# Optimization experiments

Measured on AMD Instinct MI355X. Metric: run time of the kernel, lower is better.

## Reference

```python
import jax, jax.numpy as jnp
import numpy as np

D_MODEL = 1024
NUM_HEADS = 16
D_K = D_MODEL // NUM_HEADS
THETA = 10000.0


def _apply_rope(x, positions):
    # x: [B, H, S, d_k], positions: [B, S]
    dk = x.shape[-1]
    freq = 1.0 / (THETA ** (jnp.arange(0, dk, 2, dtype=jnp.float32) / dk))  # [dk/2]
    ang = positions.astype(jnp.float32)[:, None, :, None] * freq  # [B,1,S,dk/2]
    cos, sin = jnp.cos(ang), jnp.sin(ang)
    x_even = x[..., 0::2]
    x_odd = x[..., 1::2]
    re = x_even * cos - x_odd * sin
    ro = x_even * sin + x_odd * cos
    # interleave back: [..., dk/2, 2] -> [..., dk]
    return jnp.stack([re, ro], axis=-1).reshape(x.shape)


def setup_inputs() -> dict:
    key = jax.random.key(0)
    kx, kq, kk, kv, ko = jax.random.split(key, 5)
    B, S = 2, 2048
    std = (2.0 / (D_MODEL + D_MODEL)) ** 0.5
    x = jax.random.normal(kx, (B, S, D_MODEL), dtype=jnp.float32)
    Wq = jax.random.normal(kq, (D_MODEL, D_MODEL), dtype=jnp.float32) * std
    Wk = jax.random.normal(kk, (D_MODEL, D_MODEL), dtype=jnp.float32) * std
    Wv = jax.random.normal(kv, (D_MODEL, D_MODEL), dtype=jnp.float32) * std
    Wo = jax.random.normal(ko, (D_MODEL, D_MODEL), dtype=jnp.float32) * std
    token_positions = jnp.tile(jnp.arange(S, dtype=jnp.int32)[None, :], (B, 1))
    return {"x": x, "Wq": Wq, "Wk": Wk, "Wv": Wv, "Wo": Wo,
            "token_positions": token_positions}


def reference(x, Wq, Wk, Wv, Wo, token_positions):
    B, S, D = x.shape
    H, dk = NUM_HEADS, D_K
    scale = 1.0 / np.sqrt(dk)
    # Linear is y = x @ W.T with W:[d_out, d_in]
    q = jnp.einsum('bsd,ed->bse', x, Wq).reshape(B, S, H, dk).transpose(0, 2, 1, 3)
    k = jnp.einsum('bsd,ed->bse', x, Wk).reshape(B, S, H, dk).transpose(0, 2, 1, 3)
    v = jnp.einsum('bsd,ed->bse', x, Wv).reshape(B, S, H, dk).transpose(0, 2, 1, 3)
    q = _apply_rope(q, token_positions)
    k = _apply_rope(k, token_positions)
    scores = jnp.einsum('bhqd,bhkd->bhqk', q, k) * scale  # [B,H,S,S]
    causal = jnp.tril(jnp.ones((S, S), dtype=bool))
    scores = jnp.where(causal[None, None, :, :], scores, -jnp.inf)
    probs = jax.nn.softmax(scores, axis=-1)
    attn = jnp.einsum('bhqk,bhkd->bhqd', probs, v)  # [B,H,S,dk]
    attn = attn.transpose(0, 2, 1, 3).reshape(B, S, D)
    return jnp.einsum('bsd,ed->bse', attn, Wo)
```

## Files before the change

kernel.cpp:

```cpp
#include <hip/hip_runtime.h>
#include <hip/hip_bf16.h>
#include <math.h>

#define B_  2
#define S_  2048
#define H_  16
#define D_  1024
#define DK_ 64

typedef __attribute__((ext_vector_type(8))) short bf16x8;
typedef __attribute__((ext_vector_type(8))) unsigned short ushort8v;
typedef __attribute__((ext_vector_type(4))) float f32x4;

__device__ __forceinline__ unsigned short f2bf(float f) {
  unsigned u = __float_as_uint(f);
  unsigned r = (u + 0x7FFFu + ((u >> 16) & 1u)) >> 16;
  return (unsigned short)r;
}
__device__ __forceinline__ unsigned pack_trunc(float lo, float hi) {
  return (__float_as_uint(lo) >> 16) | (__float_as_uint(hi) & 0xffff0000u);
}
__device__ __forceinline__ float fast_exp2(float x) {
#if __has_builtin(__builtin_amdgcn_exp2f)
  return __builtin_amdgcn_exp2f(x);
#else
  return __expf(x * 0.69314718056f);
#endif
}
__device__ __forceinline__ void gload_lds16(const unsigned short* g,
                                            unsigned short* l) {
  __builtin_amdgcn_global_load_lds(
      (const __attribute__((address_space(1))) unsigned int*)(const void*)g,
      (__attribute__((address_space(3))) unsigned int*)(void*)l, 16, 0, 0);
}

__global__ __launch_bounds__(256)
void cast5_bf16(const float* __restrict__ x,  const float* __restrict__ wq,
                const float* __restrict__ wk, const float* __restrict__ wv,
                const float* __restrict__ wo,
                unsigned short* __restrict__ xb,  unsigned short* __restrict__ wqb,
                unsigned short* __restrict__ wkb, unsigned short* __restrict__ wvb,
                unsigned short* __restrict__ wob)
{
  const int idx = blockIdx.x;
  const float* s; unsigned short* d; int lblk;
  if (idx < 2048) { s = x; d = xb; lblk = idx; }
  else {
    int t = idx - 2048;
    int w = t >> 9;
    lblk  = t & 511;
    s = (w == 0) ? wq  : (w == 1) ? wk  : (w == 2) ? wv  : wo;
    d = (w == 0) ? wqb : (w == 1) ? wkb : (w == 2) ? wvb : wob;
  }
  size_t i0 = ((size_t)lblk * 256 + threadIdx.x) * 8;
  float4 v0 = *(const float4*)(s + i0);
  float4 v1 = *(const float4*)(s + i0 + 4);
  ushort8v o;
  o[0] = f2bf(v0.x); o[1] = f2bf(v0.y); o[2] = f2bf(v0.z); o[3] = f2bf(v0.w);
  o[4] = f2bf(v1.x); o[5] = f2bf(v1.y); o[6] = f2bf(v1.z); o[7] = f2bf(v1.w);
  *(ushort8v*)(d + i0) = o;
}

__global__ __launch_bounds__(256)
void gemm_qkv(const unsigned short* __restrict__ A0,
              const unsigned short* __restrict__ W0,
              const unsigned short* __restrict__ W1,
              const unsigned short* __restrict__ W2,
              unsigned short* __restrict__ qh,
              unsigned short* __restrict__ kh,
              unsigned short* __restrict__ vt,
              const int* __restrict__ tp)
{
  const int z = blockIdx.z;

  const int f  = blockIdx.x + (blockIdx.y << 3);
  const int bx = (f >> 3) & 7;
  const int by = (f & 7) | ((f >> 6) << 3);

  __shared__ unsigned short As[128 * 64];
  __shared__ unsigned short Bs[128 * 64];
  __shared__ int tps[128];

  const int tid   = threadIdx.x;
  const int wave  = tid >> 6;
  const int lane  = tid & 63;
  const int quad  = lane >> 4;
  const int col16 = lane & 15;
  const int wr    = (wave >> 1) * 64;
  const int wc    = (wave & 1) * 64;

  const int row0 = (z == 2) ? bx * 128 : by * 128;
  const int col0 = (z == 2) ? by * 128 : bx * 128;
  const unsigned short* Aptr = (z == 2) ? W2 : A0;
  const unsigned short* Bptr = (z == 0) ? W0 : (z == 1) ? W1 : A0;

  if (z < 2 && tid < 128) tps[tid] = tp[row0 + tid];

  const int srow = wave * 8 + (lane >> 3);
  const int scol = ((lane & 7) ^ ((lane >> 3) & 7)) * 8;
  const unsigned short* gA = Aptr + (size_t)(row0 + srow) * D_ + scol;
  const unsigned short* gB = Bptr + (size_t)(col0 + srow) * D_ + scol;

  f32x4 acc[4][4];
  #pragma unroll
  for (int mt = 0; mt < 4; ++mt)
    #pragma unroll
    for (int nt = 0; nt < 4; ++nt)
      #pragma unroll
      for (int r = 0; r < 4; ++r) acc[mt][nt][r] = 0.f;

  for (int k0 = 0; k0 < D_; k0 += 64) {
    __syncthreads();
    #pragma unroll
    for (int p = 0; p < 4; ++p) {
      gload_lds16(gA + (size_t)(p * 32) * D_ + k0, &As[(p * 32 + wave * 8) * 64]);
      gload_lds16(gB + (size_t)(p * 32) * D_ + k0, &Bs[(p * 32 + wave * 8) * 64]);
    }
    __syncthreads();

    #pragma unroll
    for (int h = 0; h < 2; ++h) {
      const int jo = ((h * 4 + quad) ^ (col16 & 7)) * 8;
      bf16x8 af[4], bfr[4];
      #pragma unroll
      for (int mt = 0; mt < 4; ++mt)
        af[mt] = *(const bf16x8*)&As[(wr + mt * 16 + col16) * 64 + jo];
      #pragma unroll
      for (int nt = 0; nt < 4; ++nt)
        bfr[nt] = *(const bf16x8*)&Bs[(wc + nt * 16 + col16) * 64 + jo];

      #pragma unroll
      for (int mt = 0; mt < 4; ++mt)
        #pragma unroll
        for (int nt = 0; nt < 4; ++nt)
          acc[mt][nt] = __builtin_amdgcn_mfma_f32_16x16x32_bf16(
              af[mt], bfr[nt], acc[mt][nt], 0, 0, 0);
    }
  }

  if (z == 2) {
    #pragma unroll
    for (int mt = 0; mt < 4; ++mt)
      #pragma unroll
      for (int r = 0; r < 4; ++r) {
        int c = row0 + wr + mt * 16 + quad * 4 + r;
        int h = c >> 6, d = c & 63;
        #pragma unroll
        for (int nt = 0; nt < 4; ++nt) {
          int t  = col0 + wc + nt * 16 + col16;
          int bb = t >> 11, sl = t & (S_ - 1);
          vt[((size_t)((bb << 4) + h) * DK_ + d) * S_ + sl] =
              f2bf(acc[mt][nt][r]);
        }
      }
  } else {
    unsigned short* C = z ? kh : qh;
    const float qs = z ? 1.0f : 0.1803368801111204f;
    const float sgn = (col16 & 1) ? 1.f : -1.f;
    float freqr[4];
    #pragma unroll
    for (int nt = 0; nt < 4; ++nt) {
      int i = ((wc + nt * 16 + col16) & 63) >> 1;
      freqr[nt] = exp2f(-0.4152410118f * (float)i);
    }
    #pragma unroll
    for (int mt = 0; mt < 4; ++mt)
      #pragma unroll
      for (int r = 0; r < 4; ++r) {
        int rl  = wr + mt * 16 + quad * 4 + r;
        int row = row0 + rl;
        float p = (float)tps[rl];
        #pragma unroll
        for (int nt = 0; nt < 4; ++nt) {
          int col = col0 + wc + nt * 16 + col16;
          float ang = p * freqr[nt];
          float sn = __sinf(ang), cs = __cosf(ang);
          float val = acc[mt][nt][r];
          float oth = __shfl_xor(val, 1);
          C[(size_t)row * D_ + col] = f2bf((val * cs + oth * sgn * sn) * qs);
        }
      }
  }
}

__global__ __launch_bounds__(256)
void gemm_wo(const unsigned short* __restrict__ A,
             const unsigned short* __restrict__ W,
             float* __restrict__ C)
{
  __shared__ unsigned short As[64 * 64];
  __shared__ unsigned short Bs[128 * 64];

  const int f  = blockIdx.x + (blockIdx.y << 3);
  const int bx = (f >> 3) & 7;
  const int by = (f & 7) | ((f >> 6) << 3);

  const int tid   = threadIdx.x;
  const int wave  = tid >> 6;
  const int lane  = tid & 63;
  const int quad  = lane >> 4;
  const int col16 = lane & 15;
  const int row0  = by * 64;
  const int col0  = bx * 128;
  const int wr    = (wave >> 1) * 32;
  const int wc    = (wave & 1) * 64;

  const int srow = wave * 8 + (lane >> 3);
  const int scol = ((lane & 7) ^ ((lane >> 3) & 7)) * 8;
  const unsigned short* gA = A + (size_t)(row0 + srow) * D_ + scol;
  const unsigned short* gB = W + (size_t)(col0 + srow) * D_ + scol;

  f32x4 acc[2][4];
  #pragma unroll
  for (int mt = 0; mt < 2; ++mt)
    #pragma unroll
    for (int nt = 0; nt < 4; ++nt)
      #pragma unroll
      for (int r = 0; r < 4; ++r) acc[mt][nt][r] = 0.f;

  for (int k0 = 0; k0 < D_; k0 += 64) {
    __syncthreads();
    #pragma unroll
    for (int p = 0; p < 2; ++p)
      gload_lds16(gA + (size_t)(p * 32) * D_ + k0, &As[(p * 32 + wave * 8) * 64]);
    #pragma unroll
    for (int p = 0; p < 4; ++p)
      gload_lds16(gB + (size_t)(p * 32) * D_ + k0, &Bs[(p * 32 + wave * 8) * 64]);
    __syncthreads();

    #pragma unroll
    for (int h = 0; h < 2; ++h) {
      const int jo = ((h * 4 + quad) ^ (col16 & 7)) * 8;
      bf16x8 af[2], bfr[4];
      #pragma unroll
      for (int mt = 0; mt < 2; ++mt)
        af[mt] = *(const bf16x8*)&As[(wr + mt * 16 + col16) * 64 + jo];
      #pragma unroll
      for (int nt = 0; nt < 4; ++nt)
        bfr[nt] = *(const bf16x8*)&Bs[(wc + nt * 16 + col16) * 64 + jo];

      #pragma unroll
      for (int mt = 0; mt < 2; ++mt)
        #pragma unroll
        for (int nt = 0; nt < 4; ++nt)
          acc[mt][nt] = __builtin_amdgcn_mfma_f32_16x16x32_bf16(
              af[mt], bfr[nt], acc[mt][nt], 0, 0, 0);
    }
  }

  #pragma unroll
  for (int mt = 0; mt < 2; ++mt)
    #pragma unroll
    for (int r = 0; r < 4; ++r) {
      int row = row0 + wr + mt * 16 + quad * 4 + r;
      #pragma unroll
      for (int nt = 0; nt < 4; ++nt) {
        int col = col0 + wc + nt * 16 + col16;
        C[(size_t)row * D_ + col] = acc[mt][nt][r];
      }
    }
}

__device__ __forceinline__ void attn_side(
    const unsigned short* __restrict__ Ks, const unsigned short* __restrict__ Vs,
    unsigned short (* __restrict__ Pl)[72],
    const bf16x8* qf, f32x4* Oacc, float& l_i,
    int quad, int col, int qlocal, bool diag)
{
  const int jx = quad ^ (col & 7);
  f32x4 st[4];
  __builtin_amdgcn_s_setprio(1);
  #pragma unroll
  for (int nb = 0; nb < 4; ++nb) {
    const int s0 = (nb * 16 + col) * 8 + jx;
    bf16x8 ka0 = *(const bf16x8*)(Ks + s0 * 8);
    bf16x8 ka1 = *(const bf16x8*)(Ks + (s0 ^ 4) * 8);
    f32x4 a = {-24.f, -24.f, -24.f, -24.f};
    a = __builtin_amdgcn_mfma_f32_16x16x32_bf16(ka0, qf[0], a, 0, 0, 0);
    a = __builtin_amdgcn_mfma_f32_16x16x32_bf16(ka1, qf[1], a, 0, 0, 0);
    st[nb] = a;
  }
  __builtin_amdgcn_s_setprio(0);

  if (diag) {
    #pragma unroll
    for (int nb = 0; nb < 4; ++nb)
      #pragma unroll
      for (int r = 0; r < 4; ++r)
        if (nb * 16 + quad * 4 + r > qlocal) st[nb][r] = -1e30f;
  }

  float rsum = 0.f;
  #pragma unroll
  for (int nb = 0; nb < 4; ++nb)
    #pragma unroll
    for (int r = 0; r < 4; ++r) {
      float pv = fast_exp2(st[nb][r]);
      st[nb][r] = pv;
      rsum += pv;
    }
  rsum += __shfl_xor(rsum, 16);
  rsum += __shfl_xor(rsum, 32);
  l_i += rsum;

  #pragma unroll
  for (int nb = 0; nb < 4; ++nb) {
    uint2 pk;
    pk.x = pack_trunc(st[nb][0], st[nb][1]);
    pk.y = pack_trunc(st[nb][2], st[nb][3]);
    *(uint2*)&Pl[col][nb * 16 + quad * 4] = pk;
  }

  bf16x8 pf0 = *(const bf16x8*)&Pl[col][quad * 8];
  bf16x8 pf1 = *(const bf16x8*)&Pl[col][32 + quad * 8];
  __builtin_amdgcn_s_setprio(1);
  #pragma unroll
  for (int nb = 0; nb < 4; ++nb) {
    const int s0 = (nb * 16 + col) * 8 + jx;
    bf16x8 va0 = *(const bf16x8*)(Vs + s0 * 8);
    bf16x8 va1 = *(const bf16x8*)(Vs + (s0 ^ 4) * 8);
    Oacc[nb] = __builtin_amdgcn_mfma_f32_16x16x32_bf16(va0, pf0, Oacc[nb], 0, 0, 0);
    Oacc[nb] = __builtin_amdgcn_mfma_f32_16x16x32_bf16(va1, pf1, Oacc[nb], 0, 0, 0);
  }
  __builtin_amdgcn_s_setprio(0);
}

__global__ __launch_bounds__(256)
void attn_mfma(const unsigned short* __restrict__ Q,
               const unsigned short* __restrict__ K,
               const unsigned short* __restrict__ Vt,
               unsigned short* __restrict__ O)
{
  const int f    = blockIdx.x + (blockIdx.y << 4);
  const int qtA  = (f >> 3) & 15;
  const int bh   = (f & 7) | ((f >> 7) << 3);
  const int qtB  = 31 - qtA;
  const int b    = bh >> 4, h = bh & 15;
  const int tid  = threadIdx.x;
  const int wave = tid >> 6;
  const int lane = tid & 63;
  const int quad = lane >> 4;
  const int col  = lane & 15;
  const int qlocal = wave * 16 + col;

  __shared__ unsigned short Ks[1024 * 8];
  __shared__ unsigned short Vs[1024 * 8];
  __shared__ unsigned short PlA[4][16][72];
  __shared__ unsigned short PlB[4][16][72];

  const size_t qkbase = (size_t)b * S_ * D_ + (size_t)h * DK_;
  const size_t vtbase = (size_t)bh * DK_ * S_;

  const int qrowA = qtA * 64 + qlocal;
  const int qrowB = qtB * 64 + qlocal;
  bf16x8 qfA[2], qfB[2];
  qfA[0] = *(const bf16x8*)(Q + qkbase + (size_t)qrowA * D_ + quad * 8);
  qfA[1] = *(const bf16x8*)(Q + qkbase + (size_t)qrowA * D_ + 32 + quad * 8);
  qfB[0] = *(const bf16x8*)(Q + qkbase + (size_t)qrowB * D_ + quad * 8);
  qfB[1] = *(const bf16x8*)(Q + qkbase + (size_t)qrowB * D_ + 32 + quad * 8);

  const int sr = tid >> 3;
  const int sj = (tid & 7) ^ (sr & 7);
  const unsigned short* gK = K + qkbase + (size_t)sr * D_ + sj * 8;
  const unsigned short* gV = Vt + vtbase + (size_t)sr * S_ + sj * 8;

  f32x4 OaccA[4], OaccB[4];
  #pragma unroll
  for (int nb = 0; nb < 4; ++nb)
    #pragma unroll
    for (int r = 0; r < 4; ++r) { OaccA[nb][r] = 0.f; OaccB[nb][r] = 0.f; }
  float lA = 0.f, lB = 0.f;

  const int nH = qtB + 1;

  auto stage = [&](int g) {
    const int kbase = g << 6;
    unsigned short* Kd = Ks + (g & 1) * 4096 + wave * 512;
    unsigned short* Vd = Vs + (g & 1) * 4096 + wave * 512;
    #pragma unroll
    for (int p = 0; p < 2; ++p) {
      gload_lds16(gK + (size_t)(kbase + p * 32) * D_, Kd + p * 2048);
      gload_lds16(gV + (size_t)(p * 32) * S_ + kbase, Vd + p * 2048);
    }
  };

  stage(0);

  for (int g = 0; g < nH; ++g) {
    if (g + 1 < nH) {
      stage(g + 1);
      asm volatile("s_waitcnt vmcnt(4)" ::: "memory");
    } else {
      asm volatile("s_waitcnt vmcnt(0)" ::: "memory");
    }
    __builtin_amdgcn_s_barrier();
    __builtin_amdgcn_sched_barrier(0);

    const unsigned short* KsH = Ks + (g & 1) * 4096;
    const unsigned short* VsH = Vs + (g & 1) * 4096;
    attn_side(KsH, VsH, PlB[wave], qfB, OaccB, lB, quad, col, qlocal,
              g == qtB);
    if (g <= qtA)
      attn_side(KsH, VsH, PlA[wave], qfA, OaccA, lA, quad, col, qlocal,
                g == qtA);

    __builtin_amdgcn_sched_barrier(0);
    __builtin_amdgcn_s_barrier();
  }

  const float invA = 1.0f / lA;
  const float invB = 1.0f / lB;
  #pragma unroll
  for (int nb = 0; nb < 4; ++nb) {
    int d = nb * 16 + quad * 4;
    ushort4 oa, ob;
    oa.x = f2bf(OaccA[nb][0] * invA); oa.y = f2bf(OaccA[nb][1] * invA);
    oa.z = f2bf(OaccA[nb][2] * invA); oa.w = f2bf(OaccA[nb][3] * invA);
    ob.x = f2bf(OaccB[nb][0] * invB); ob.y = f2bf(OaccB[nb][1] * invB);
    ob.z = f2bf(OaccB[nb][2] * invB); ob.w = f2bf(OaccB[nb][3] * invB);
    *(ushort4*)(O + (size_t)b * S_ * D_ + (size_t)qrowA * D_ + h * DK_ + d) = oa;
    *(ushort4*)(O + (size_t)b * S_ * D_ + (size_t)qrowB * D_ + h * DK_ + d) = ob;
  }
}

extern "C" void kernel_launch(void* const* d_in, const int* in_sizes, int n_in,
                              void* d_out, int out_size, void* d_ws, size_t ws_size,
                              hipStream_t stream)
{
  const float* x  = (const float*)d_in[0];
  const float* Wq = (const float*)d_in[1];
  const float* Wk = (const float*)d_in[2];
  const float* Wv = (const float*)d_in[3];
  const float* Wo = (const float*)d_in[4];
  const int*   tp = (const int*)d_in[5];
  float* out = (float*)d_out;

  const size_t NTOK = (size_t)B_ * S_ * D_;
  const size_t NW   = (size_t)D_ * D_;
  unsigned short* qh  = (unsigned short*)d_ws;
  unsigned short* kh  = qh + NTOK;
  unsigned short* vt  = kh + NTOK;
  unsigned short* xb  = vt + NTOK;
  unsigned short* wqb = xb + NTOK;
  unsigned short* wkb = wqb + NW;
  unsigned short* wvb = wkb + NW;
  unsigned short* wob = wvb + NW;
  unsigned short* ab  = xb;

  cast5_bf16<<<dim3(4096), 256, 0, stream>>>(
      x, Wq, Wk, Wv, Wo, xb, wqb, wkb, wvb, wob);

  gemm_qkv<<<dim3(D_ / 128, (B_ * S_) / 128, 3), 256, 0, stream>>>(
      xb, wqb, wkb, wvb, qh, kh, vt, tp);

  attn_mfma<<<dim3(16, B_ * H_), 256, 0, stream>>>(qh, kh, vt, ab);

  gemm_wo<<<dim3(D_ / 128, (B_ * S_) / 64), 256, 0, stream>>>(ab, wob, out);
}
```

Before: 180.3 us.

## Split attention KV range across two wave groups per query tile

Replaces the paired-query-tile scheme (each 256-thread block handling two complementary 64-row tiles) with one query tile per 512-thread block. The block's two 4-wave groups take even and odd KV tiles and merge partial outputs and row sums through LDS at the end. The grid grows from 512 to 1024 blocks, launched longest tiles first, to improve occupancy and load balance. In exchange it adds more barriers per iteration, staged K/V loads spread across barrier phases, idle waves on the odd final tile, and a final LDS reduction.

```diff
diff --git a/kernel.cpp b/kernel.cpp
--- a/kernel.cpp
+++ b/kernel.cpp
@@ -261,165 +261,187 @@
     }
 }
 
-__device__ __forceinline__ void attn_side(
-    const unsigned short* __restrict__ Ks, const unsigned short* __restrict__ Vs,
-    unsigned short (* __restrict__ Pl)[72],
-    const bf16x8* qf, f32x4* Oacc, float& l_i,
-    int quad, int col, int qlocal, bool diag)
-{
-  const int jx = quad ^ (col & 7);
-  f32x4 st[4];
-  __builtin_amdgcn_s_setprio(1);
-  #pragma unroll
-  for (int nb = 0; nb < 4; ++nb) {
-    const int s0 = (nb * 16 + col) * 8 + jx;
-    bf16x8 ka0 = *(const bf16x8*)(Ks + s0 * 8);
-    bf16x8 ka1 = *(const bf16x8*)(Ks + (s0 ^ 4) * 8);
-    f32x4 a = {-24.f, -24.f, -24.f, -24.f};
-    a = __builtin_amdgcn_mfma_f32_16x16x32_bf16(ka0, qf[0], a, 0, 0, 0);
-    a = __builtin_amdgcn_mfma_f32_16x16x32_bf16(ka1, qf[1], a, 0, 0, 0);
-    st[nb] = a;
-  }
-  __builtin_amdgcn_s_setprio(0);
-
-  if (diag) {
-    #pragma unroll
-    for (int nb = 0; nb < 4; ++nb)
-      #pragma unroll
-      for (int r = 0; r < 4; ++r)
-        if (nb * 16 + quad * 4 + r > qlocal) st[nb][r] = -1e30f;
-  }
-
-  float rsum = 0.f;
-  #pragma unroll
-  for (int nb = 0; nb < 4; ++nb)
-    #pragma unroll
-    for (int r = 0; r < 4; ++r) {
-      float pv = fast_exp2(st[nb][r]);
-      st[nb][r] = pv;
-      rsum += pv;
-    }
-  rsum += __shfl_xor(rsum, 16);
-  rsum += __shfl_xor(rsum, 32);
-  l_i += rsum;
-
-  #pragma unroll
-  for (int nb = 0; nb < 4; ++nb) {
-    uint2 pk;
-    pk.x = pack_trunc(st[nb][0], st[nb][1]);
-    pk.y = pack_trunc(st[nb][2], st[nb][3]);
-    *(uint2*)&Pl[col][nb * 16 + quad * 4] = pk;
-  }
-
-  bf16x8 pf0 = *(const bf16x8*)&Pl[col][quad * 8];
-  bf16x8 pf1 = *(const bf16x8*)&Pl[col][32 + quad * 8];
-  __builtin_amdgcn_s_setprio(1);
-  #pragma unroll
-  for (int nb = 0; nb < 4; ++nb) {
-    const int s0 = (nb * 16 + col) * 8 + jx;
-    bf16x8 va0 = *(const bf16x8*)(Vs + s0 * 8);
-    bf16x8 va1 = *(const bf16x8*)(Vs + (s0 ^ 4) * 8);
-    Oacc[nb] = __builtin_amdgcn_mfma_f32_16x16x32_bf16(va0, pf0, Oacc[nb], 0, 0, 0);
-    Oacc[nb] = __builtin_amdgcn_mfma_f32_16x16x32_bf16(va1, pf1, Oacc[nb], 0, 0, 0);
-  }
-  __builtin_amdgcn_s_setprio(0);
-}
-
-__global__ __launch_bounds__(256)
+__global__ __launch_bounds__(512, 6)
 void attn_mfma(const unsigned short* __restrict__ Q,
                const unsigned short* __restrict__ K,
                const unsigned short* __restrict__ Vt,
                unsigned short* __restrict__ O)
 {
-  const int f    = blockIdx.x + (blockIdx.y << 4);
-  const int qtA  = (f >> 3) & 15;
-  const int bh   = (f & 7) | ((f >> 7) << 3);
-  const int qtB  = 31 - qtA;
-  const int b    = bh >> 4, h = bh & 15;
+  const int f   = blockIdx.x;
+  const int qt  = 31 - (f >> 5);
+  const int bh  = f & 31;
+  const int b   = bh >> 4, h = bh & 15;
+
   const int tid  = threadIdx.x;
-  const int wave = tid >> 6;
+  const int w    = tid >> 6;
   const int lane = tid & 63;
   const int quad = lane >> 4;
   const int col  = lane & 15;
-  const int qlocal = wave * 16 + col;
-
-  __shared__ unsigned short Ks[1024 * 8];
-  __shared__ unsigned short Vs[1024 * 8];
-  __shared__ unsigned short PlA[4][16][72];
-  __shared__ unsigned short PlB[4][16][72];
+  const int rw   = w & 3;
+  const int p    = w >> 2;
+  const int qlocal = rw * 16 + col;
+
+  __shared__ unsigned short Ks[2 * 4096];
+  __shared__ unsigned short Vs[2 * 4096];
+  __shared__ __align__(16) unsigned short Pl[8][16][72];
 
   const size_t qkbase = (size_t)b * S_ * D_ + (size_t)h * DK_;
   const size_t vtbase = (size_t)bh * DK_ * S_;
 
-  const int qrowA = qtA * 64 + qlocal;
-  const int qrowB = qtB * 64 + qlocal;
-  bf16x8 qfA[2], qfB[2];
-  qfA[0] = *(const bf16x8*)(Q + qkbase + (size_t)qrowA * D_ + quad * 8);
-  qfA[1] = *(const bf16x8*)(Q + qkbase + (size_t)qrowA * D_ + 32 + quad * 8);
-  qfB[0] = *(const bf16x8*)(Q + qkbase + (size_t)qrowB * D_ + quad * 8);
-  qfB[1] = *(const bf16x8*)(Q + qkbase + (size_t)qrowB * D_ + 32 + quad * 8);
-
-  const int sr = tid >> 3;
-  const int sj = (tid & 7) ^ (sr & 7);
-  const unsigned short* gK = K + qkbase + (size_t)sr * D_ + sj * 8;
-  const unsigned short* gV = Vt + vtbase + (size_t)sr * S_ + sj * 8;
-
-  f32x4 OaccA[4], OaccB[4];
+  const int qrow = qt * 64 + qlocal;
+  bf16x8 qf[2];
+  qf[0] = *(const bf16x8*)(Q + qkbase + (size_t)qrow * D_ + quad * 8);
+  qf[1] = *(const bf16x8*)(Q + qkbase + (size_t)qrow * D_ + 32 + quad * 8);
+
+  const int lr8 = lane >> 3;
+  const int sj  = ((lane & 7) ^ (lr8 & 7)) * 8;
+
+  auto stageK = [&](int g) {
+    const int gc = (g > qt) ? qt : g;
+    const unsigned short* s =
+        K + qkbase + (size_t)(gc * 64 + rw * 16 + lr8) * D_ + sj;
+    #pragma unroll
+    for (int pp = 0; pp < 2; ++pp)
+      gload_lds16(s + (size_t)(pp * 8) * D_, &Ks[p * 4096 + (rw * 16 + pp * 8) * 64]);
+  };
+  auto stageV = [&](int g) {
+    const int gc = (g > qt) ? qt : g;
+    const unsigned short* s =
+        Vt + vtbase + (size_t)(rw * 16 + lr8) * S_ + gc * 64 + sj;
+    #pragma unroll
+    for (int pp = 0; pp < 2; ++pp)
+      gload_lds16(s + (size_t)(pp * 8) * S_, &Vs[p * 4096 + (rw * 16 + pp * 8) * 64]);
+  };
+
+  f32x4 Oacc[4];
   #pragma unroll
   for (int nb = 0; nb < 4; ++nb)
     #pragma unroll
-    for (int r = 0; r < 4; ++r) { OaccA[nb][r] = 0.f; OaccB[nb][r] = 0.f; }
-  float lA = 0.f, lB = 0.f;
-
-  const int nH = qtB + 1;
-
-  auto stage = [&](int g) {
-    const int kbase = g << 6;
-    unsigned short* Kd = Ks + (g & 1) * 4096 + wave * 512;
-    unsigned short* Vd = Vs + (g & 1) * 4096 + wave * 512;
-    #pragma unroll
-    for (int p = 0; p < 2; ++p) {
-      gload_lds16(gK + (size_t)(kbase + p * 32) * D_, Kd + p * 2048);
-      gload_lds16(gV + (size_t)(p * 32) * S_ + kbase, Vd + p * 2048);
-    }
-  };
-
-  stage(0);
-
-  for (int g = 0; g < nH; ++g) {
-    if (g + 1 < nH) {
-      stage(g + 1);
-      asm volatile("s_waitcnt vmcnt(4)" ::: "memory");
-    } else {
-      asm volatile("s_waitcnt vmcnt(0)" ::: "memory");
-    }
+    for (int r = 0; r < 4; ++r) Oacc[nb][r] = 0.f;
+  float l_i = 0.f;
+
+  const int M  = (qt >> 1) + 1;
+  const int jx = quad ^ (col & 7);
+  const unsigned short* KsH = Ks + p * 4096;
+  const unsigned short* VsH = Vs + p * 4096;
+  unsigned short (*Plw)[72] = Pl[w];
+
+  stageK(p);
+  stageV(p);
+  asm volatile("s_waitcnt vmcnt(0)" ::: "memory");
+  __builtin_amdgcn_s_barrier();
+  __builtin_amdgcn_sched_barrier(0);
+
+  for (int m = 0; m < M; ++m) {
+    const int g    = 2 * m + p;
+    const bool act = (g <= qt);
+    const bool dg  = (g == qt);
+
+    f32x4 st[4];
+    if (act) {
+      __builtin_amdgcn_s_setprio(1);
+      #pragma unroll
+      for (int nb = 0; nb < 4; ++nb) {
+        const int s0 = (nb * 16 + col) * 8 + jx;
+        bf16x8 ka0 = *(const bf16x8*)(KsH + s0 * 8);
+        bf16x8 ka1 = *(const bf16x8*)(KsH + (s0 ^ 4) * 8);
+        f32x4 a = {-24.f, -24.f, -24.f, -24.f};
+        a = __builtin_amdgcn_mfma_f32_16x16x32_bf16(ka0, qf[0], a, 0, 0, 0);
+        a = __builtin_amdgcn_mfma_f32_16x16x32_bf16(ka1, qf[1], a, 0, 0, 0);
+        st[nb] = a;
+      }
+      __builtin_amdgcn_s_setprio(0);
+    }
+    __builtin_amdgcn_sched_barrier(0);
     __builtin_amdgcn_s_barrier();
     __builtin_amdgcn_sched_barrier(0);
 
-    const unsigned short* KsH = Ks + (g & 1) * 4096;
-    const unsigned short* VsH = Vs + (g & 1) * 4096;
-    attn_side(KsH, VsH, PlB[wave], qfB, OaccB, lB, quad, col, qlocal,
-              g == qtB);
-    if (g <= qtA)
-      attn_side(KsH, VsH, PlA[wave], qfA, OaccA, lA, quad, col, qlocal,
-                g == qtA);
-
+    stageK(2 * m + 2 + p);
+
+    if (act) {
+      if (dg) {
+        #pragma unroll
+        for (int nb = 0; nb < 4; ++nb)
+          #pragma unroll
+          for (int r = 0; r < 4; ++r)
+            if (nb * 16 + quad * 4 + r > qlocal) st[nb][r] = -1e30f;
+      }
+      float rsum = 0.f;
+      #pragma unroll
+      for (int nb = 0; nb < 4; ++nb)
+        #pragma unroll
+        for (int r = 0; r < 4; ++r) {
+          float pv = fast_exp2(st[nb][r]);
+          st[nb][r] = pv;
+          rsum += pv;
+        }
+      rsum += __shfl_xor(rsum, 16);
+      rsum += __shfl_xor(rsum, 32);
+      l_i += rsum;
+      #pragma unroll
+      for (int nb = 0; nb < 4; ++nb) {
+        uint2 pk;
+        pk.x = pack_trunc(st[nb][0], st[nb][1]);
+        pk.y = pack_trunc(st[nb][2], st[nb][3]);
+        *(uint2*)&Plw[col][nb * 16 + quad * 4] = pk;
+      }
+    }
+
+    asm volatile("s_waitcnt vmcnt(2)" ::: "memory");
     __builtin_amdgcn_sched_barrier(0);
     __builtin_amdgcn_s_barrier();
-  }
-
-  const float invA = 1.0f / lA;
-  const float invB = 1.0f / lB;
-  #pragma unroll
-  for (int nb = 0; nb < 4; ++nb) {
-    int d = nb * 16 + quad * 4;
-    ushort4 oa, ob;
-    oa.x = f2bf(OaccA[nb][0] * invA); oa.y = f2bf(OaccA[nb][1] * invA);
-    oa.z = f2bf(OaccA[nb][2] * invA); oa.w = f2bf(OaccA[nb][3] * invA);
-    ob.x = f2bf(OaccB[nb][0] * invB); ob.y = f2bf(OaccB[nb][1] * invB);
-    ob.z = f2bf(OaccB[nb][2] * invB); ob.w = f2bf(OaccB[nb][3] * invB);
-    *(ushort4*)(O + (size_t)b * S_ * D_ + (size_t)qrowA * D_ + h * DK_ + d) = oa;
-    *(ushort4*)(O + (size_t)b * S_ * D_ + (size_t)qrowB * D_ + h * DK_ + d) = ob;
+    __builtin_amdgcn_sched_barrier(0);
+
+    if (act) {
+      bf16x8 pf0 = *(const bf16x8*)&Plw[col][quad * 8];
+      bf16x8 pf1 = *(const bf16x8*)&Plw[col][32 + quad * 8];
+      __builtin_amdgcn_s_setprio(1);
+      #pragma unroll
+      for (int nb = 0; nb < 4; ++nb) {
+        const int s0 = (nb * 16 + col) * 8 + jx;
+        bf16x8 va0 = *(const bf16x8*)(VsH + s0 * 8);
+        bf16x8 va1 = *(const bf16x8*)(VsH + (s0 ^ 4) * 8);
+        Oacc[nb] = __builtin_amdgcn_mfma_f32_16x16x32_bf16(va0, pf0, Oacc[nb], 0, 0, 0);
+        Oacc[nb] = __builtin_amdgcn_mfma_f32_16x16x32_bf16(va1, pf1, Oacc[nb], 0, 0, 0);
+      }
+      __builtin_amdgcn_s_setprio(0);
+    }
+    __builtin_amdgcn_sched_barrier(0);
+    __builtin_amdgcn_s_barrier();
+    __builtin_amdgcn_sched_barrier(0);
+
+    stageV(2 * m + 2 + p);
+    asm volatile("s_waitcnt vmcnt(2)" ::: "memory");
+    __builtin_amdgcn_sched_barrier(0);
+    __builtin_amdgcn_s_barrier();
+    __builtin_amdgcn_sched_barrier(0);
+  }
+
+  asm volatile("s_waitcnt vmcnt(0)" ::: "memory");
+  __syncthreads();
+  float* sc = (float*)&Pl[0][0][0];
+  if (p == 1) {
+    float* d0 = sc + ((size_t)(rw * 64 + lane)) * 18;
+    #pragma unroll
+    for (int nb = 0; nb < 4; ++nb)
+      #pragma unroll
+      for (int r = 0; r < 4; ++r) d0[nb * 4 + r] = Oacc[nb][r];
+    d0[16] = l_i;
+  }
+  __syncthreads();
+  if (p == 0) {
+    const float* s0 = sc + ((size_t)(rw * 64 + lane)) * 18;
+    const float inv = 1.0f / (l_i + s0[16]);
+    #pragma unroll
+    for (int nb = 0; nb < 4; ++nb) {
+      int d = nb * 16 + quad * 4;
+      ushort4 oa;
+      oa.x = f2bf((Oacc[nb][0] + s0[nb * 4 + 0]) * inv);
+      oa.y = f2bf((Oacc[nb][1] + s0[nb * 4 + 1]) * inv);
+      oa.z = f2bf((Oacc[nb][2] + s0[nb * 4 + 2]) * inv);
+      oa.w = f2bf((Oacc[nb][3] + s0[nb * 4 + 3]) * inv);
+      *(ushort4*)(O + (size_t)b * S_ * D_ + (size_t)qrow * D_ + h * DK_ + d) = oa;
+    }
   }
 }
 
@@ -453,7 +475,7 @@
   gemm_qkv<<<dim3(D_ / 128, (B_ * S_) / 128, 3), 256, 0, stream>>>(
       xb, wqb, wkb, wvb, qh, kh, vt, tp);
 
-  attn_mfma<<<dim3(16, B_ * H_), 256, 0, stream>>>(qh, kh, vt, ab);
+  attn_mfma<<<dim3(32 * 32), 512, 0, stream>>>(qh, kh, vt, ab);
 
   gemm_wo<<<dim3(D_ / 128, (B_ * S_) / 64), 256, 0, stream>>>(ab, wob, out);
 }
```

New measurement: 171.4 us. 4.9% less time.
